# Kernel tuning notes

Measured on AMD Instinct MI355X. Metric: run time of the kernel, lower is better.

## Reference

```python
import jax, jax.numpy as jnp
import numpy as np

N = 100000
E = 1600000
NEG_SLOPE = 0.2


def _param(key, shape, scale=0.05):
    return jax.random.normal(key, shape, dtype=jnp.float32) * scale


def setup_inputs() -> dict:
    key = jax.random.key(0)
    ks = jax.random.split(key, 16)
    x = jax.random.normal(ks[0], (N, 128), dtype=jnp.float32)
    edge_index = jax.random.randint(ks[1], (2, E), 0, N, dtype=jnp.int64)
    # layer 1: 128 -> (H=2, C=64), concat
    W1 = _param(ks[2], (128, 2 * 64)); a_src1 = _param(ks[3], (2, 64)); a_dst1 = _param(ks[4], (2, 64)); b1 = jnp.zeros((128,), jnp.float32)
    # layer 2: 128 -> (H=2, C=64), concat
    W2 = _param(ks[5], (128, 2 * 64)); a_src2 = _param(ks[6], (2, 64)); a_dst2 = _param(ks[7], (2, 64)); b2 = jnp.zeros((128,), jnp.float32)
    # layer 3: 128 -> (H=1, C=64), mean (concat=False)
    W3 = _param(ks[8], (128, 1 * 64)); a_src3 = _param(ks[9], (1, 64)); a_dst3 = _param(ks[10], (1, 64)); b3 = jnp.zeros((64,), jnp.float32)
    return {"x": x, "edge_index": edge_index,
            "W1": W1, "a_src1": a_src1, "a_dst1": a_dst1, "b1": b1,
            "W2": W2, "a_src2": a_src2, "a_dst2": a_dst2, "b2": b2,
            "W3": W3, "a_src3": a_src3, "a_dst3": a_dst3, "b3": b3}


def gat_layer(x, src, dst, W, a_src, a_dst, b, concat):
    H, C = a_src.shape
    n = x.shape[0]
    h = (x @ W).reshape(n, H, C)                      # [N,H,C]
    # per-node attention logits (avoid [E,H,C] gather for the score step)
    al_s = jnp.sum(h * a_src[None], axis=-1)          # [N,H]
    al_d = jnp.sum(h * a_dst[None], axis=-1)          # [N,H]
    e = al_s[src] + al_d[dst]                         # [E',H]
    e = jnp.where(e > 0, e, NEG_SLOPE * e)            # LeakyReLU(0.2)
    # scatter-softmax over incoming edges per destination node
    m = jax.ops.segment_max(e, dst, num_segments=n)   # [N,H]
    ex = jnp.exp(e - m[dst])
    z = jax.ops.segment_sum(ex, dst, num_segments=n)  # [N,H]
    alpha = ex / z[dst]                               # [E',H]
    msg = h[src] * alpha[:, :, None]                  # [E',H,C]
    out = jax.ops.segment_sum(msg, dst, num_segments=n)  # [N,H,C]
    out = out.reshape(n, H * C) if concat else out.mean(axis=1)
    return out + b


def reference(x, edge_index, W1, a_src1, a_dst1, b1, W2, a_src2, a_dst2, b2, W3, a_src3, a_dst3, b3):
    n = x.shape[0]
    loop = jnp.arange(n, dtype=edge_index.dtype)
    src = jnp.concatenate([edge_index[0], loop])      # add self-loops (PyG default)
    dst = jnp.concatenate([edge_index[1], loop])
    h = gat_layer(x, src, dst, W1, a_src1, a_dst1, b1, True)
    h = jax.nn.relu(h)
    h = gat_layer(h, src, dst, W2, a_src2, a_dst2, b2, True)
    h = jax.nn.relu(h)
    return gat_layer(h, src, dst, W3, a_src3, a_dst3, b3, False)
```

## Files before the change

kernel.cpp:

```cpp
#include <hip/hip_runtime.h>

#define NEG_SLOPE 0.2f
#define BUK_SHIFT 9
#define BUK_SIZE 512
#define BUK_CAP 16384

typedef unsigned short u16;
typedef __attribute__((ext_vector_type(4))) float f4v;
typedef _Float16 h8 __attribute__((ext_vector_type(8)));

__device__ __forceinline__ u16 f2h_bits(_Float16 h) {
    union { _Float16 f; u16 u; } c;
    c.f = h;
    return c.u;
}


__device__ __forceinline__ void load_split_f32(const float* __restrict__ X, int row,
                                               int koff, int N, h8& hi, h8& lo) {
    float v[8];
    if (row < N) {
        float4 a = *(const float4*)&X[(size_t)row * 128 + koff];
        float4 b = *(const float4*)&X[(size_t)row * 128 + koff + 4];
        v[0] = a.x; v[1] = a.y; v[2] = a.z; v[3] = a.w;
        v[4] = b.x; v[5] = b.y; v[6] = b.z; v[7] = b.w;
    } else {
#pragma unroll
        for (int i = 0; i < 8; i++) v[i] = 0.f;
    }
    union { h8 s; _Float16 u[8]; } H, L;
#pragma unroll
    for (int i = 0; i < 8; i++) {
        H.u[i] = (_Float16)v[i];
        L.u[i] = (_Float16)(v[i] - (float)H.u[i]);
    }
    hi = H.s;
    lo = L.s;
}

template <int M, bool FP32X>
__device__ __forceinline__ void gemm_body(int gb, const float* __restrict__ Xf,
                                          const u16* __restrict__ XH,
                                          const u16* __restrict__ WTh,
                                          const u16* __restrict__ WTl,
                                          _Float16* __restrict__ Hout,
                                          float* __restrict__ als,
                                          float* __restrict__ ald, int nrows) {
    const int CT = M / 16;
    const int CTX = CT + 1;
    const int H = (M == 128) ? 2 : 1;
    int tid = threadIdx.x;
    int wv = tid >> 6, lane = tid & 63;
    int q = lane >> 4, nl = lane & 15;
    int R0 = gb * 256 + wv * 32;
    int rt0 = R0 >> 4;

    f4v acc[2][CTX];
    f4v z4 = {0.f, 0.f, 0.f, 0.f};
#pragma unroll
    for (int rt = 0; rt < 2; rt++)
#pragma unroll
        for (int ct = 0; ct < CTX; ct++) acc[rt][ct] = z4;

#pragma unroll
    for (int ch = 0; ch < 4; ch++) {
        h8 ah0, al0, ah1, al1;
        if (FP32X) {
            int koff = ch * 32 + q * 8;
            load_split_f32(Xf, R0 + nl, koff, nrows, ah0, al0);
            load_split_f32(Xf, R0 + 16 + nl, koff, nrows, ah1, al1);
        } else {
            size_t a0 = ((size_t)rt0 * 4 + ch) * 512 + lane * 8;
            size_t a1 = ((size_t)(rt0 + 1) * 4 + ch) * 512 + lane * 8;
            ah0 = *(const h8*)&XH[a0];
            ah1 = *(const h8*)&XH[a1];
        }
#pragma unroll
        for (int ct = 0; ct < CTX; ct++) {
            size_t bb = ((size_t)ct * 4 + ch) * 512 + lane * 8;
            h8 bh = *(const h8*)&WTh[bb];
            h8 bl = *(const h8*)&WTl[bb];
            acc[0][ct] = __builtin_amdgcn_mfma_f32_16x16x32_f16(ah0, bh, acc[0][ct], 0, 0, 0);
            acc[0][ct] = __builtin_amdgcn_mfma_f32_16x16x32_f16(ah0, bl, acc[0][ct], 0, 0, 0);
            acc[1][ct] = __builtin_amdgcn_mfma_f32_16x16x32_f16(ah1, bh, acc[1][ct], 0, 0, 0);
            acc[1][ct] = __builtin_amdgcn_mfma_f32_16x16x32_f16(ah1, bl, acc[1][ct], 0, 0, 0);
            if (FP32X) {
                acc[0][ct] = __builtin_amdgcn_mfma_f32_16x16x32_f16(al0, bh, acc[0][ct], 0, 0, 0);
                acc[1][ct] = __builtin_amdgcn_mfma_f32_16x16x32_f16(al1, bh, acc[1][ct], 0, 0, 0);
            }
        }
    }

#pragma unroll
    for (int rt = 0; rt < 2; rt++)
#pragma unroll
        for (int ct = 0; ct < CT; ct++)
#pragma unroll
            for (int r = 0; r < 4; r++) {
                int row = R0 + rt * 16 + q * 4 + r;
                if (row < nrows) Hout[(size_t)row * M + ct * 16 + nl] = (_Float16)acc[rt][ct][r];
            }

    if (nl < 2 * H) {
#pragma unroll
        for (int rt = 0; rt < 2; rt++)
#pragma unroll
            for (int r = 0; r < 4; r++) {
                int row = R0 + rt * 16 + q * 4 + r;
                if (row < nrows) {
                    float v = acc[rt][CT][r];
                    if (H == 2) {
                        float* dstp = (nl < 2) ? als : ald;
                        dstp[(size_t)row * 2 + (nl & 1)] = v;
                    } else {
                        float* dstp = (nl == 0) ? als : ald;
                        dstp[row] = v;
                    }
                }
            }
    }
}

template <int M, bool FP32X>
__launch_bounds__(512)
__global__ void k_gemm(const float* __restrict__ Xf, const u16* __restrict__ XH,
                       const u16* __restrict__ WTh, const u16* __restrict__ WTl,
                       _Float16* __restrict__ Hout, float* __restrict__ als,
                       float* __restrict__ ald, int nrows) {
    gemm_body<M, FP32X>(blockIdx.x, Xf, XH, WTh, WTl, Hout, als, ald, nrows);
}


__launch_bounds__(512)
__global__ void k_d1(const int* __restrict__ ei, int* g_cnt, int* buckets, int E, int nb,
                     int nbin, const float* __restrict__ W1, const float* __restrict__ as1,
                     const float* __restrict__ ad1, const float* __restrict__ W2,
                     const float* __restrict__ as2, const float* __restrict__ ad2,
                     const float* __restrict__ W3, const float* __restrict__ as3,
                     const float* __restrict__ ad3, u16* __restrict__ T1h,
                     u16* __restrict__ T1l, u16* __restrict__ T2h, u16* __restrict__ T2l,
                     u16* __restrict__ T3h, u16* __restrict__ T3l) {
    __shared__ int lcnt[256], lbase[256], lcur[256];
    int b = blockIdx.x;
    int t = threadIdx.x;
    if (b < nbin) {
        if (t < nb) {
            lcnt[t] = 0;
            lcur[t] = 0;
        }
        __syncthreads();
        int tile0 = b * 4096;
        int pk[8], bk[8];
#pragma unroll
        for (int k = 0; k < 8; k++) {
            int idx = tile0 + k * 512 + t;
            bk[k] = -1;
            if (idx < E) {
                int s = ei[idx];
                int d = ei[E + idx];
                bk[k] = d >> BUK_SHIFT;
                pk[k] = (s << BUK_SHIFT) | (d & (BUK_SIZE - 1));
                atomicAdd(&lcnt[bk[k]], 1);
            }
        }
        __syncthreads();
        if (t < nb && lcnt[t] > 0) lbase[t] = atomicAdd(&g_cnt[t], lcnt[t]);
        __syncthreads();
#pragma unroll
        for (int k = 0; k < 8; k++) {
            if (bk[k] >= 0) {
                int p = lbase[bk[k]] + atomicAdd(&lcur[bk[k]], 1);
                if (p < BUK_CAP) buckets[(bk[k] << 14) + p] = pk[k];
            }
        }
        return;
    }
    int rb = b - nbin;
    if (rb < 80) {
        int idx = rb * 512 + t;
        const float* W;
        u16 *Th, *Tl;
        int M, li;
        if (idx < 16384) {
            W = W1; Th = T1h; Tl = T1l; M = 128; li = idx;
        } else if (idx < 32768) {
            W = W2; Th = T2h; Tl = T2l; M = 128; li = idx - 16384;
        } else {
            W = W3; Th = T3h; Tl = T3l; M = 64; li = idx - 32768;
        }
        int c = li >> 7, k = li & 127;
        float v = W[(size_t)k * M + c];
        _Float16 h = (_Float16)v;
        _Float16 l = (_Float16)(v - (float)h);
        int ct = c >> 4, ch = k >> 5, q = (k >> 3) & 3, j = k & 7;
        size_t addr = ((size_t)ct * 4 + ch) * 512 + ((c & 15) + 16 * q) * 8 + j;
        Th[addr] = f2h_bits(h);
        Tl[addr] = f2h_bits(l);
    } else {
        int idx = (rb - 80) * 512 + t;
        if (idx >= 6144) return;
        int layer = idx >> 11;
        int rem = idx & 2047;
        int k = rem >> 4;
        int c = rem & 15;
        const float *W, *as, *ad;
        u16 *Th, *Tl;
        int M, CT, nc;
        if (layer == 0) {
            W = W1; as = as1; ad = ad1; Th = T1h; Tl = T1l; M = 128; CT = 8; nc = 4;
        } else if (layer == 1) {
            W = W2; as = as2; ad = ad2; Th = T2h; Tl = T2l; M = 128; CT = 8; nc = 4;
        } else {
            W = W3; as = as3; ad = ad3; Th = T3h; Tl = T3l; M = 64; CT = 4; nc = 2;
        }
        float val = 0.f;
        if (c < nc) {
            int side, hh;
            if (nc == 4) { side = c >> 1; hh = c & 1; }
            else { side = c; hh = 0; }
            const float* a = side ? ad : as;
            for (int j = 0; j < 64; j++)
                val += W[(size_t)k * M + hh * 64 + j] * a[hh * 64 + j];
        }
        _Float16 h = (_Float16)val;
        _Float16 l = (_Float16)(val - (float)h);
        int ch = k >> 5, q = (k >> 3) & 3, j = k & 7;
        size_t addr = ((size_t)CT * 4 + ch) * 512 + ((size_t)(c + 16 * q)) * 8 + j;
        Th[addr] = f2h_bits(h);
        Tl[addr] = f2h_bits(l);
    }
}


__launch_bounds__(512)
__global__ void k_d2(const int* __restrict__ g_cnt, const int* __restrict__ buckets,
                     int* csr_ptr, int* csr_src, int n, int nb,
                     const float* __restrict__ x, const u16* __restrict__ WTh,
                     const u16* __restrict__ WTl, _Float16* __restrict__ Hout,
                     float* __restrict__ als, float* __restrict__ ald) {
    __shared__ int lcnt[512], lsc[512], lcur[512], bsc[512];
    int b = blockIdx.x;
    int t = threadIdx.x;
    if (b >= nb) {
        gemm_body<128, true>(b - nb, x, nullptr, WTh, WTl, Hout, als, ald, n);
        return;
    }
    int nodes = min(BUK_SIZE, n - b * BUK_SIZE);
    int cnt = min(g_cnt[b], BUK_CAP);
    const int* bp = &buckets[b << 14];

    int bv = 0;
    if (t < nb) bv = min(g_cnt[t], BUK_CAP) + min(BUK_SIZE, n - t * BUK_SIZE);
    bsc[t] = bv;
    __syncthreads();
    for (int off = 1; off < 512; off <<= 1) {
        int xx = (t >= off) ? bsc[t - off] : 0;
        __syncthreads();
        bsc[t] += xx;
        __syncthreads();
    }
    int boff = bsc[b] - (cnt + nodes);
    int total = bsc[nb - 1];
    __syncthreads();

    lcnt[t] = 0;
    __syncthreads();
    for (int i = t; i < cnt; i += 512) atomicAdd(&lcnt[bp[i] & (BUK_SIZE - 1)], 1);
    __syncthreads();
    int myc = (t < nodes) ? (lcnt[t] + 1) : 0;
    lsc[t] = myc;
    __syncthreads();
    for (int off = 1; off < 512; off <<= 1) {
        int xx = (t >= off) ? lsc[t - off] : 0;
        __syncthreads();
        lsc[t] += xx;
        __syncthreads();
    }
    int excl = lsc[t] - myc;
    lcur[t] = excl;
    if (t < nodes) csr_ptr[b * BUK_SIZE + t] = boff + excl;
    if (b == nb - 1 && t == 0) csr_ptr[n] = total;
    __syncthreads();
    for (int i = t; i < cnt; i += 512) {
        int v = bp[i];
        int ld = v & (BUK_SIZE - 1);
        int p = atomicAdd(&lcur[ld], 1);
        csr_src[boff + p] = v >> BUK_SHIFT;
    }
    if (t < nodes) {
        int p = atomicAdd(&lcur[t], 1);
        csr_src[boff + p] = b * BUK_SIZE + t;
    }
}


__launch_bounds__(256)
__global__ void k_agg128(const int* __restrict__ ptr, const int* __restrict__ srcv,
                         const _Float16* __restrict__ Hh, const float* __restrict__ als,
                         const float* __restrict__ ald, const float* __restrict__ bias,
                         u16* __restrict__ OutX, int n) {
    int wvg = (blockIdx.x * blockDim.x + threadIdx.x) >> 6;
    int lane = threadIdx.x & 63;
    int nn = lane >> 4;
    int gl = lane & 15;
    int wid = wvg * 4 + nn;
    bool valid = wid < n;
    int widc = valid ? wid : (n - 1);
    int start = ptr[widc];
    int deg = valid ? (ptr[widc + 1] - start) : 0;
    int md = deg;
    md = max(md, __shfl_xor(md, 16));
    md = max(md, __shfl_xor(md, 32));
    float2 adv = *(const float2*)&ald[(size_t)widc * 2];
    int hsel = gl >> 3;
    int coff = gl * 8;
    float z0 = 0.f, z1 = 0.f;
    float acc[8];
#pragma unroll
    for (int c = 0; c < 8; c++) acc[c] = 0.f;

    for (int base = 0; base < md; base += 16) {
        int i = base + gl;
        int s_l = 0;
        float ex0 = 0.f, ex1 = 0.f;
        if (i < deg) {
            s_l = srcv[start + i];
            float2 av = *(const float2*)&als[(size_t)s_l * 2];
            float e0 = av.x + adv.x;
            e0 = e0 > 0.f ? e0 : NEG_SLOPE * e0;
            ex0 = __expf(e0);
            float e1 = av.y + adv.y;
            e1 = e1 > 0.f ? e1 : NEG_SLOPE * e1;
            ex1 = __expf(e1);
        }
        z0 += ex0;
        z1 += ex1;
        int cnt = min(16, md - base);
        for (int jp = 0; jp < cnt; jp += 4) {
            int nk = min(4, cnt - jp);
            h8 hv[4];
            float w[4];
#pragma unroll
            for (int k = 0; k < 4; k++) {
                if (k < nk) {
                    int j = nn * 16 + jp + k;
                    int s = __shfl(s_l, j);
                    float w0 = __shfl(ex0, j);
                    float w1 = __shfl(ex1, j);
                    w[k] = hsel ? w1 : w0;
                    hv[k] = *(const h8*)&Hh[(size_t)s * 128 + coff];
                }
            }
#pragma unroll
            for (int k = 0; k < 4; k++) {
                if (k < nk) {
#pragma unroll
                    for (int c = 0; c < 8; c++)
                        acc[c] = fmaf(w[k], (float)hv[k][c], acc[c]);
                }
            }
        }
    }

#pragma unroll
    for (int m = 1; m <= 8; m <<= 1) {
        z0 += __shfl_xor(z0, m);
        z1 += __shfl_xor(z1, m);
    }
    if (valid) {
        float zinv = hsel ? (1.f / z1) : (1.f / z0);
        float4 b0 = *(const float4*)&bias[coff];
        float4 b1 = *(const float4*)&bias[coff + 4];
        float bb[8] = {b0.x, b0.y, b0.z, b0.w, b1.x, b1.y, b1.z, b1.w};
        union { _Float16 f[8]; h8 v; } O;
#pragma unroll
        for (int c = 0; c < 8; c++) {
            float o = fmaxf(fmaf(acc[c], zinv, bb[c]), 0.f);
            O.f[c] = (_Float16)o;
        }
        int ch = coff >> 5, qq = (coff >> 3) & 3;
        size_t tb = ((size_t)(wid >> 4) * 4 + ch) * 512 + ((size_t)((wid & 15) + 16 * qq)) * 8;
        *(h8*)&OutX[tb] = O.v;
    }
}


__launch_bounds__(256)
__global__ void k_agg64(const int* __restrict__ ptr, const int* __restrict__ srcv,
                        const _Float16* __restrict__ Hh, const float* __restrict__ als,
                        const float* __restrict__ ald, const float* __restrict__ bias,
                        float* __restrict__ Out, int n) {
    int wvg = (blockIdx.x * blockDim.x + threadIdx.x) >> 6;
    int lane = threadIdx.x & 63;
    int nn = lane >> 3;
    int gl = lane & 7;
    int wid = wvg * 8 + nn;
    bool valid = wid < n;
    int widc = valid ? wid : (n - 1);
    int start = ptr[widc];
    int deg = valid ? (ptr[widc + 1] - start) : 0;
    int md = deg;
    md = max(md, __shfl_xor(md, 8));
    md = max(md, __shfl_xor(md, 16));
    md = max(md, __shfl_xor(md, 32));
    float ad0 = ald[widc];
    int coff = gl * 8;
    float z = 0.f;
    float acc[8];
#pragma unroll
    for (int c = 0; c < 8; c++) acc[c] = 0.f;

    for (int base = 0; base < md; base += 8) {
        int i = base + gl;
        int s_l = 0;
        float ex0 = 0.f;
        if (i < deg) {
            s_l = srcv[start + i];
            float e = als[s_l] + ad0;
            e = e > 0.f ? e : NEG_SLOPE * e;
            ex0 = __expf(e);
        }
        z += ex0;
        int cnt = min(8, md - base);
        for (int jp = 0; jp < cnt; jp += 4) {
            int nk = min(4, cnt - jp);
            h8 hv[4];
            float w[4];
#pragma unroll
            for (int k = 0; k < 4; k++) {
                if (k < nk) {
                    int j = nn * 8 + jp + k;
                    int s = __shfl(s_l, j);
                    w[k] = __shfl(ex0, j);
                    hv[k] = *(const h8*)&Hh[(size_t)s * 64 + coff];
                }
            }
#pragma unroll
            for (int k = 0; k < 4; k++) {
                if (k < nk) {
#pragma unroll
                    for (int c = 0; c < 8; c++)
                        acc[c] = fmaf(w[k], (float)hv[k][c], acc[c]);
                }
            }
        }
    }

#pragma unroll
    for (int m = 1; m <= 4; m <<= 1) z += __shfl_xor(z, m);
    if (valid) {
        float zinv = 1.f / z;
        float4 b0 = *(const float4*)&bias[coff];
        float4 b1 = *(const float4*)&bias[coff + 4];
        float4 o1, o2;
        o1.x = fmaf(acc[0], zinv, b0.x);
        o1.y = fmaf(acc[1], zinv, b0.y);
        o1.z = fmaf(acc[2], zinv, b0.z);
        o1.w = fmaf(acc[3], zinv, b0.w);
        o2.x = fmaf(acc[4], zinv, b1.x);
        o2.y = fmaf(acc[5], zinv, b1.y);
        o2.z = fmaf(acc[6], zinv, b1.z);
        o2.w = fmaf(acc[7], zinv, b1.w);
        *(float4*)&Out[(size_t)wid * 64 + coff] = o1;
        *(float4*)&Out[(size_t)wid * 64 + coff + 4] = o2;
    }
}


extern "C" void kernel_launch(void* const* d_in, const int* in_sizes, int n_in,
                              void* d_out, int out_size, void* d_ws, size_t ws_size,
                              hipStream_t stream) {
    const float* x = (const float*)d_in[0];
    const int* ei = (const int*)d_in[1];
    const float* W1 = (const float*)d_in[2];
    const float* as1 = (const float*)d_in[3];
    const float* ad1 = (const float*)d_in[4];
    const float* b1 = (const float*)d_in[5];
    const float* W2 = (const float*)d_in[6];
    const float* as2 = (const float*)d_in[7];
    const float* ad2 = (const float*)d_in[8];
    const float* b2 = (const float*)d_in[9];
    const float* W3 = (const float*)d_in[10];
    const float* as3 = (const float*)d_in[11];
    const float* ad3 = (const float*)d_in[12];
    const float* b3 = (const float*)d_in[13];

    const int N = in_sizes[0] / 128;
    const int E = in_sizes[1] / 2;
    const int NB = (N + BUK_SIZE - 1) / BUK_SIZE;
    const int Npad = (N + 255) & ~255;

    char* p = (char*)d_ws;
    auto alloc = [&](size_t bytes) -> char* {
        char* r = p;
        p += (bytes + 255) & ~(size_t)255;
        return r;
    };
    int* g_cnt = (int*)alloc(256 * 4);
    int* buckets = (int*)alloc((size_t)NB * BUK_CAP * 4);
    int* csr_ptr = (int*)alloc((size_t)(N + 1) * 4);
    int* csr_src = (int*)alloc((size_t)(E + N) * 4);
    float* als = (float*)alloc((size_t)N * 2 * 4);
    float* aldv = (float*)alloc((size_t)N * 2 * 4);
    _Float16* Hbuf = (_Float16*)alloc((size_t)N * 128 * 2);
    u16* XH = (u16*)alloc((size_t)Npad * 128 * 2);
    u16* WT1h = (u16*)alloc(9 * 2048 * 2);
    u16* WT1l = (u16*)alloc(9 * 2048 * 2);
    u16* WT2h = (u16*)alloc(9 * 2048 * 2);
    u16* WT2l = (u16*)alloc(9 * 2048 * 2);
    u16* WT3h = (u16*)alloc(5 * 2048 * 2);
    u16* WT3l = (u16*)alloc(5 * 2048 * 2);

    const int GTOT = Npad / 256;
    const int NBIN = (E + 4095) / 4096;
    const int waves128 = (N + 3) / 4;
    const int nbAgg128 = (waves128 + 3) / 4;
    const int waves64 = (N + 7) / 8;
    const int nbAgg64 = (waves64 + 3) / 4;

    hipMemsetAsync(g_cnt, 0, 256 * 4, stream);

    k_d1<<<NBIN + 92, 512, 0, stream>>>(ei, g_cnt, buckets, E, NB, NBIN,
                                        W1, as1, ad1, W2, as2, ad2, W3, as3, ad3,
                                        WT1h, WT1l, WT2h, WT2l, WT3h, WT3l);

    k_d2<<<NB + GTOT, 512, 0, stream>>>(g_cnt, buckets, csr_ptr, csr_src, N, NB,
                                        x, WT1h, WT1l, Hbuf, als, aldv);

    k_agg128<<<nbAgg128, 256, 0, stream>>>(csr_ptr, csr_src, Hbuf, als, aldv, b1, XH, N);

    k_gemm<128, false><<<GTOT, 512, 0, stream>>>(nullptr, XH, WT2h, WT2l,
                                                 Hbuf, als, aldv, N);
    k_agg128<<<nbAgg128, 256, 0, stream>>>(csr_ptr, csr_src, Hbuf, als, aldv, b2, XH, N);

    k_gemm<64, false><<<GTOT, 512, 0, stream>>>(nullptr, XH, WT3h, WT3l,
                                                Hbuf, als, aldv, N);
    k_agg64<<<nbAgg64, 256, 0, stream>>>(csr_ptr, csr_src, Hbuf, als, aldv, b3,
                                         (float*)d_out, N);
}
```

Measured before the change: 400.5 us.

## Fuse all GAT stages into one cooperative persistent kernel with grid syncs

Replaces the memset and seven separate launches with a single cooperative kernel that loops over virtual blocks for each stage and uses grid.sync between stages, falling back to per-stage kernels if the cooperative launch fails. This targets launch overhead and inter-kernel gaps. The aggregation kernels are also recast as 512-thread blocks, and the gather inner loop is widened from 4 to 8 neighbours per batch. The risks are lower occupancy from the merged kernel's register and LDS footprint, grid-sync costs, and load imbalance across the persistent grid.

```diff
diff --git a/kernel.cpp b/kernel.cpp
--- a/kernel.cpp
+++ b/kernel.cpp
@@ -1,4 +1,7 @@
 #include <hip/hip_runtime.h>
+#include <hip/hip_cooperative_groups.h>
+
+namespace cg = cooperative_groups;
 
 #define NEG_SLOPE 0.2f
 #define BUK_SHIFT 9
@@ -9,10 +12,172 @@
 typedef __attribute__((ext_vector_type(4))) float f4v;
 typedef _Float16 h8 __attribute__((ext_vector_type(8)));
 
+struct MegaP {
+    const float* x;
+    const int* ei;
+    const float *W1, *as1, *ad1, *b1;
+    const float *W2, *as2, *ad2, *b2;
+    const float *W3, *as3, *ad3, *b3;
+    float* out;
+    int N, E, NB, NBIN, GTOT, VB128, VB64;
+    int *g_cnt, *buckets, *csr_ptr, *csr_src;
+    float *als, *ald;
+    _Float16* Hbuf;
+    u16* XH;
+    u16 *WT1h, *WT1l, *WT2h, *WT2l, *WT3h, *WT3l;
+};
+
 __device__ __forceinline__ u16 f2h_bits(_Float16 h) {
     union { _Float16 f; u16 u; } c;
     c.f = h;
     return c.u;
+}
+
+
+__device__ void wsplit_role(const MegaP& p, int idx) {
+    const float* W;
+    u16 *Th, *Tl;
+    int M, li;
+    if (idx < 16384) {
+        W = p.W1; Th = p.WT1h; Tl = p.WT1l; M = 128; li = idx;
+    } else if (idx < 32768) {
+        W = p.W2; Th = p.WT2h; Tl = p.WT2l; M = 128; li = idx - 16384;
+    } else {
+        W = p.W3; Th = p.WT3h; Tl = p.WT3l; M = 64; li = idx - 32768;
+    }
+    int c = li >> 7, k = li & 127;
+    float v = W[(size_t)k * M + c];
+    _Float16 h = (_Float16)v;
+    _Float16 l = (_Float16)(v - (float)h);
+    int ct = c >> 4, ch = k >> 5, q = (k >> 3) & 3, j = k & 7;
+    size_t addr = ((size_t)ct * 4 + ch) * 512 + ((c & 15) + 16 * q) * 8 + j;
+    Th[addr] = f2h_bits(h);
+    Tl[addr] = f2h_bits(l);
+}
+
+__device__ void wa_role(const MegaP& p, int idx) {
+    if (idx >= 6144) return;
+    int layer = idx >> 11;
+    int rem = idx & 2047;
+    int k = rem >> 4;
+    int c = rem & 15;
+    const float *W, *as, *ad;
+    u16 *Th, *Tl;
+    int M, CT, nc;
+    if (layer == 0) {
+        W = p.W1; as = p.as1; ad = p.ad1; Th = p.WT1h; Tl = p.WT1l; M = 128; CT = 8; nc = 4;
+    } else if (layer == 1) {
+        W = p.W2; as = p.as2; ad = p.ad2; Th = p.WT2h; Tl = p.WT2l; M = 128; CT = 8; nc = 4;
+    } else {
+        W = p.W3; as = p.as3; ad = p.ad3; Th = p.WT3h; Tl = p.WT3l; M = 64; CT = 4; nc = 2;
+    }
+    float val = 0.f;
+    if (c < nc) {
+        int side, hh;
+        if (nc == 4) { side = c >> 1; hh = c & 1; }
+        else { side = c; hh = 0; }
+        const float* a = side ? ad : as;
+        for (int j = 0; j < 64; j++)
+            val += W[(size_t)k * M + hh * 64 + j] * a[hh * 64 + j];
+    }
+    _Float16 h = (_Float16)val;
+    _Float16 l = (_Float16)(val - (float)h);
+    int ch = k >> 5, q = (k >> 3) & 3, j = k & 7;
+    size_t addr = ((size_t)CT * 4 + ch) * 512 + ((size_t)(c + 16 * q)) * 8 + j;
+    Th[addr] = f2h_bits(h);
+    Tl[addr] = f2h_bits(l);
+}
+
+__device__ void binscatter_role(const MegaP& p, int b, int t, int* smem) {
+    int* lcnt = smem;
+    int* lbase = smem + 256;
+    int* lcur = smem + 512;
+    int nb = p.NB;
+    if (t < nb) {
+        lcnt[t] = 0;
+        lcur[t] = 0;
+    }
+    __syncthreads();
+    int tile0 = b * 4096;
+    int pk[8], bk[8];
+#pragma unroll
+    for (int k = 0; k < 8; k++) {
+        int idx = tile0 + k * 512 + t;
+        bk[k] = -1;
+        if (idx < p.E) {
+            int s = p.ei[idx];
+            int d = p.ei[p.E + idx];
+            bk[k] = d >> BUK_SHIFT;
+            pk[k] = (s << BUK_SHIFT) | (d & (BUK_SIZE - 1));
+            atomicAdd(&lcnt[bk[k]], 1);
+        }
+    }
+    __syncthreads();
+    if (t < nb && lcnt[t] > 0) lbase[t] = atomicAdd(&p.g_cnt[t], lcnt[t]);
+    __syncthreads();
+#pragma unroll
+    for (int k = 0; k < 8; k++) {
+        if (bk[k] >= 0) {
+            int pos = lbase[bk[k]] + atomicAdd(&lcur[bk[k]], 1);
+            if (pos < BUK_CAP) p.buckets[(bk[k] << 14) + pos] = pk[k];
+        }
+    }
+    __syncthreads();
+}
+
+__device__ void csr_role(const MegaP& p, int b, int t, int* smem) {
+    int* lcnt = smem;
+    int* lsc = smem + 512;
+    int* lcur = smem + 1024;
+    int* bsc = smem + 1536;
+    int n = p.N, nb = p.NB;
+    int nodes = min(BUK_SIZE, n - b * BUK_SIZE);
+    int cnt = min(p.g_cnt[b], BUK_CAP);
+    const int* bp = &p.buckets[b << 14];
+
+    int bv = 0;
+    if (t < nb) bv = min(p.g_cnt[t], BUK_CAP) + min(BUK_SIZE, n - t * BUK_SIZE);
+    bsc[t] = bv;
+    __syncthreads();
+    for (int off = 1; off < 512; off <<= 1) {
+        int xx = (t >= off) ? bsc[t - off] : 0;
+        __syncthreads();
+        bsc[t] += xx;
+        __syncthreads();
+    }
+    int boff = bsc[b] - (cnt + nodes);
+    int total = bsc[nb - 1];
+    __syncthreads();
+
+    lcnt[t] = 0;
+    __syncthreads();
+    for (int i = t; i < cnt; i += 512) atomicAdd(&lcnt[bp[i] & (BUK_SIZE - 1)], 1);
+    __syncthreads();
+    int myc = (t < nodes) ? (lcnt[t] + 1) : 0;
+    lsc[t] = myc;
+    __syncthreads();
+    for (int off = 1; off < 512; off <<= 1) {
+        int xx = (t >= off) ? lsc[t - off] : 0;
+        __syncthreads();
+        lsc[t] += xx;
+        __syncthreads();
+    }
+    int excl = lsc[t] - myc;
+    lcur[t] = excl;
+    if (t < nodes) p.csr_ptr[b * BUK_SIZE + t] = boff + excl;
+    if (b == nb - 1 && t == 0) p.csr_ptr[n] = total;
+    __syncthreads();
+    for (int i = t; i < cnt; i += 512) {
+        int v = bp[i];
+        int ld = v & (BUK_SIZE - 1);
+        int pos = atomicAdd(&lcur[ld], 1);
+        p.csr_src[boff + pos] = v >> BUK_SHIFT;
+    }
+    if (t < nodes) {
+        int pos = atomicAdd(&lcur[t], 1);
+        p.csr_src[boff + pos] = b * BUK_SIZE + t;
+    }
+    __syncthreads();
 }
 
 
@@ -39,13 +204,10 @@
 }
 
 template <int M, bool FP32X>
-__device__ __forceinline__ void gemm_body(int gb, const float* __restrict__ Xf,
-                                          const u16* __restrict__ XH,
-                                          const u16* __restrict__ WTh,
-                                          const u16* __restrict__ WTl,
-                                          _Float16* __restrict__ Hout,
-                                          float* __restrict__ als,
-                                          float* __restrict__ ald, int nrows) {
+__device__ void gemm_body(int gb, const float* __restrict__ Xf, const u16* __restrict__ XH,
+                          const u16* __restrict__ WTh, const u16* __restrict__ WTl,
+                          _Float16* __restrict__ Hout, float* __restrict__ als,
+                          float* __restrict__ ald, int nrows) {
     const int CT = M / 16;
     const int CTX = CT + 1;
     const int H = (M == 128) ? 2 : 1;
@@ -121,197 +283,22 @@
     }
 }
 
-template <int M, bool FP32X>
-__launch_bounds__(512)
-__global__ void k_gemm(const float* __restrict__ Xf, const u16* __restrict__ XH,
-                       const u16* __restrict__ WTh, const u16* __restrict__ WTl,
-                       _Float16* __restrict__ Hout, float* __restrict__ als,
-                       float* __restrict__ ald, int nrows) {
-    gemm_body<M, FP32X>(blockIdx.x, Xf, XH, WTh, WTl, Hout, als, ald, nrows);
-}
-
-
-__launch_bounds__(512)
-__global__ void k_d1(const int* __restrict__ ei, int* g_cnt, int* buckets, int E, int nb,
-                     int nbin, const float* __restrict__ W1, const float* __restrict__ as1,
-                     const float* __restrict__ ad1, const float* __restrict__ W2,
-                     const float* __restrict__ as2, const float* __restrict__ ad2,
-                     const float* __restrict__ W3, const float* __restrict__ as3,
-                     const float* __restrict__ ad3, u16* __restrict__ T1h,
-                     u16* __restrict__ T1l, u16* __restrict__ T2h, u16* __restrict__ T2l,
-                     u16* __restrict__ T3h, u16* __restrict__ T3l) {
-    __shared__ int lcnt[256], lbase[256], lcur[256];
-    int b = blockIdx.x;
-    int t = threadIdx.x;
-    if (b < nbin) {
-        if (t < nb) {
-            lcnt[t] = 0;
-            lcur[t] = 0;
-        }
-        __syncthreads();
-        int tile0 = b * 4096;
-        int pk[8], bk[8];
-#pragma unroll
-        for (int k = 0; k < 8; k++) {
-            int idx = tile0 + k * 512 + t;
-            bk[k] = -1;
-            if (idx < E) {
-                int s = ei[idx];
-                int d = ei[E + idx];
-                bk[k] = d >> BUK_SHIFT;
-                pk[k] = (s << BUK_SHIFT) | (d & (BUK_SIZE - 1));
-                atomicAdd(&lcnt[bk[k]], 1);
-            }
-        }
-        __syncthreads();
-        if (t < nb && lcnt[t] > 0) lbase[t] = atomicAdd(&g_cnt[t], lcnt[t]);
-        __syncthreads();
-#pragma unroll
-        for (int k = 0; k < 8; k++) {
-            if (bk[k] >= 0) {
-                int p = lbase[bk[k]] + atomicAdd(&lcur[bk[k]], 1);
-                if (p < BUK_CAP) buckets[(bk[k] << 14) + p] = pk[k];
-            }
-        }
-        return;
-    }
-    int rb = b - nbin;
-    if (rb < 80) {
-        int idx = rb * 512 + t;
-        const float* W;
-        u16 *Th, *Tl;
-        int M, li;
-        if (idx < 16384) {
-            W = W1; Th = T1h; Tl = T1l; M = 128; li = idx;
-        } else if (idx < 32768) {
-            W = W2; Th = T2h; Tl = T2l; M = 128; li = idx - 16384;
-        } else {
-            W = W3; Th = T3h; Tl = T3l; M = 64; li = idx - 32768;
-        }
-        int c = li >> 7, k = li & 127;
-        float v = W[(size_t)k * M + c];
-        _Float16 h = (_Float16)v;
-        _Float16 l = (_Float16)(v - (float)h);
-        int ct = c >> 4, ch = k >> 5, q = (k >> 3) & 3, j = k & 7;
-        size_t addr = ((size_t)ct * 4 + ch) * 512 + ((c & 15) + 16 * q) * 8 + j;
-        Th[addr] = f2h_bits(h);
-        Tl[addr] = f2h_bits(l);
-    } else {
-        int idx = (rb - 80) * 512 + t;
-        if (idx >= 6144) return;
-        int layer = idx >> 11;
-        int rem = idx & 2047;
-        int k = rem >> 4;
-        int c = rem & 15;
-        const float *W, *as, *ad;
-        u16 *Th, *Tl;
-        int M, CT, nc;
-        if (layer == 0) {
-            W = W1; as = as1; ad = ad1; Th = T1h; Tl = T1l; M = 128; CT = 8; nc = 4;
-        } else if (layer == 1) {
-            W = W2; as = as2; ad = ad2; Th = T2h; Tl = T2l; M = 128; CT = 8; nc = 4;
-        } else {
-            W = W3; as = as3; ad = ad3; Th = T3h; Tl = T3l; M = 64; CT = 4; nc = 2;
-        }
-        float val = 0.f;
-        if (c < nc) {
-            int side, hh;
-            if (nc == 4) { side = c >> 1; hh = c & 1; }
-            else { side = c; hh = 0; }
-            const float* a = side ? ad : as;
-            for (int j = 0; j < 64; j++)
-                val += W[(size_t)k * M + hh * 64 + j] * a[hh * 64 + j];
-        }
-        _Float16 h = (_Float16)val;
-        _Float16 l = (_Float16)(val - (float)h);
-        int ch = k >> 5, q = (k >> 3) & 3, j = k & 7;
-        size_t addr = ((size_t)CT * 4 + ch) * 512 + ((size_t)(c + 16 * q)) * 8 + j;
-        Th[addr] = f2h_bits(h);
-        Tl[addr] = f2h_bits(l);
-    }
-}
-
-
-__launch_bounds__(512)
-__global__ void k_d2(const int* __restrict__ g_cnt, const int* __restrict__ buckets,
-                     int* csr_ptr, int* csr_src, int n, int nb,
-                     const float* __restrict__ x, const u16* __restrict__ WTh,
-                     const u16* __restrict__ WTl, _Float16* __restrict__ Hout,
-                     float* __restrict__ als, float* __restrict__ ald) {
-    __shared__ int lcnt[512], lsc[512], lcur[512], bsc[512];
-    int b = blockIdx.x;
-    int t = threadIdx.x;
-    if (b >= nb) {
-        gemm_body<128, true>(b - nb, x, nullptr, WTh, WTl, Hout, als, ald, n);
-        return;
-    }
-    int nodes = min(BUK_SIZE, n - b * BUK_SIZE);
-    int cnt = min(g_cnt[b], BUK_CAP);
-    const int* bp = &buckets[b << 14];
-
-    int bv = 0;
-    if (t < nb) bv = min(g_cnt[t], BUK_CAP) + min(BUK_SIZE, n - t * BUK_SIZE);
-    bsc[t] = bv;
-    __syncthreads();
-    for (int off = 1; off < 512; off <<= 1) {
-        int xx = (t >= off) ? bsc[t - off] : 0;
-        __syncthreads();
-        bsc[t] += xx;
-        __syncthreads();
-    }
-    int boff = bsc[b] - (cnt + nodes);
-    int total = bsc[nb - 1];
-    __syncthreads();
-
-    lcnt[t] = 0;
-    __syncthreads();
-    for (int i = t; i < cnt; i += 512) atomicAdd(&lcnt[bp[i] & (BUK_SIZE - 1)], 1);
-    __syncthreads();
-    int myc = (t < nodes) ? (lcnt[t] + 1) : 0;
-    lsc[t] = myc;
-    __syncthreads();
-    for (int off = 1; off < 512; off <<= 1) {
-        int xx = (t >= off) ? lsc[t - off] : 0;
-        __syncthreads();
-        lsc[t] += xx;
-        __syncthreads();
-    }
-    int excl = lsc[t] - myc;
-    lcur[t] = excl;
-    if (t < nodes) csr_ptr[b * BUK_SIZE + t] = boff + excl;
-    if (b == nb - 1 && t == 0) csr_ptr[n] = total;
-    __syncthreads();
-    for (int i = t; i < cnt; i += 512) {
-        int v = bp[i];
-        int ld = v & (BUK_SIZE - 1);
-        int p = atomicAdd(&lcur[ld], 1);
-        csr_src[boff + p] = v >> BUK_SHIFT;
-    }
-    if (t < nodes) {
-        int p = atomicAdd(&lcur[t], 1);
-        csr_src[boff + p] = b * BUK_SIZE + t;
-    }
-}
-
-
-__launch_bounds__(256)
-__global__ void k_agg128(const int* __restrict__ ptr, const int* __restrict__ srcv,
-                         const _Float16* __restrict__ Hh, const float* __restrict__ als,
-                         const float* __restrict__ ald, const float* __restrict__ bias,
-                         u16* __restrict__ OutX, int n) {
-    int wvg = (blockIdx.x * blockDim.x + threadIdx.x) >> 6;
-    int lane = threadIdx.x & 63;
+
+__device__ void agg128_role(const MegaP& p, int t, int vb, const float* __restrict__ bias) {
+    int wv = t >> 6, lane = t & 63;
+    int wvg = vb * 8 + wv;
+    if (wvg * 4 >= p.N) return;
     int nn = lane >> 4;
     int gl = lane & 15;
     int wid = wvg * 4 + nn;
-    bool valid = wid < n;
-    int widc = valid ? wid : (n - 1);
-    int start = ptr[widc];
-    int deg = valid ? (ptr[widc + 1] - start) : 0;
+    bool valid = wid < p.N;
+    int widc = valid ? wid : (p.N - 1);
+    int start = p.csr_ptr[widc];
+    int deg = valid ? (p.csr_ptr[widc + 1] - start) : 0;
     int md = deg;
     md = max(md, __shfl_xor(md, 16));
     md = max(md, __shfl_xor(md, 32));
-    float2 adv = *(const float2*)&ald[(size_t)widc * 2];
+    float2 adv = *(const float2*)&p.ald[(size_t)widc * 2];
     int hsel = gl >> 3;
     int coff = gl * 8;
     float z0 = 0.f, z1 = 0.f;
@@ -324,8 +311,8 @@
         int s_l = 0;
         float ex0 = 0.f, ex1 = 0.f;
         if (i < deg) {
-            s_l = srcv[start + i];
-            float2 av = *(const float2*)&als[(size_t)s_l * 2];
+            s_l = p.csr_src[start + i];
+            float2 av = *(const float2*)&p.als[(size_t)s_l * 2];
             float e0 = av.x + adv.x;
             e0 = e0 > 0.f ? e0 : NEG_SLOPE * e0;
             ex0 = __expf(e0);
@@ -336,23 +323,23 @@
         z0 += ex0;
         z1 += ex1;
         int cnt = min(16, md - base);
-        for (int jp = 0; jp < cnt; jp += 4) {
-            int nk = min(4, cnt - jp);
-            h8 hv[4];
-            float w[4];
-#pragma unroll
-            for (int k = 0; k < 4; k++) {
+        for (int jp = 0; jp < cnt; jp += 8) {
+            int nk = min(8, cnt - jp);
+            h8 hv[8];
+            float w[8];
+#pragma unroll
+            for (int k = 0; k < 8; k++) {
                 if (k < nk) {
                     int j = nn * 16 + jp + k;
                     int s = __shfl(s_l, j);
                     float w0 = __shfl(ex0, j);
                     float w1 = __shfl(ex1, j);
                     w[k] = hsel ? w1 : w0;
-                    hv[k] = *(const h8*)&Hh[(size_t)s * 128 + coff];
+                    hv[k] = *(const h8*)&p.Hbuf[(size_t)s * 128 + coff];
                 }
             }
 #pragma unroll
-            for (int k = 0; k < 4; k++) {
+            for (int k = 0; k < 8; k++) {
                 if (k < nk) {
 #pragma unroll
                     for (int c = 0; c < 8; c++)
@@ -380,30 +367,26 @@
         }
         int ch = coff >> 5, qq = (coff >> 3) & 3;
         size_t tb = ((size_t)(wid >> 4) * 4 + ch) * 512 + ((size_t)((wid & 15) + 16 * qq)) * 8;
-        *(h8*)&OutX[tb] = O.v;
-    }
-}
-
-
-__launch_bounds__(256)
-__global__ void k_agg64(const int* __restrict__ ptr, const int* __restrict__ srcv,
-                        const _Float16* __restrict__ Hh, const float* __restrict__ als,
-                        const float* __restrict__ ald, const float* __restrict__ bias,
-                        float* __restrict__ Out, int n) {
-    int wvg = (blockIdx.x * blockDim.x + threadIdx.x) >> 6;
-    int lane = threadIdx.x & 63;
+        *(h8*)&p.XH[tb] = O.v;
+    }
+}
+
+__device__ void agg64_role(const MegaP& p, int t, int vb) {
+    int wv = t >> 6, lane = t & 63;
+    int wvg = vb * 8 + wv;
+    if (wvg * 8 >= p.N) return;
     int nn = lane >> 3;
     int gl = lane & 7;
     int wid = wvg * 8 + nn;
-    bool valid = wid < n;
-    int widc = valid ? wid : (n - 1);
-    int start = ptr[widc];
-    int deg = valid ? (ptr[widc + 1] - start) : 0;
+    bool valid = wid < p.N;
+    int widc = valid ? wid : (p.N - 1);
+    int start = p.csr_ptr[widc];
+    int deg = valid ? (p.csr_ptr[widc + 1] - start) : 0;
     int md = deg;
     md = max(md, __shfl_xor(md, 8));
     md = max(md, __shfl_xor(md, 16));
     md = max(md, __shfl_xor(md, 32));
-    float ad0 = ald[widc];
+    float ad0 = p.ald[widc];
     int coff = gl * 8;
     float z = 0.f;
     float acc[8];
@@ -415,33 +398,30 @@
         int s_l = 0;
         float ex0 = 0.f;
         if (i < deg) {
-            s_l = srcv[start + i];
-            float e = als[s_l] + ad0;
+            s_l = p.csr_src[start + i];
+            float e = p.als[s_l] + ad0;
             e = e > 0.f ? e : NEG_SLOPE * e;
             ex0 = __expf(e);
         }
         z += ex0;
         int cnt = min(8, md - base);
-        for (int jp = 0; jp < cnt; jp += 4) {
-            int nk = min(4, cnt - jp);
-            h8 hv[4];
-            float w[4];
-#pragma unroll
-            for (int k = 0; k < 4; k++) {
-                if (k < nk) {
-                    int j = nn * 8 + jp + k;
-                    int s = __shfl(s_l, j);
-                    w[k] = __shfl(ex0, j);
-                    hv[k] = *(const h8*)&Hh[(size_t)s * 64 + coff];
-                }
+        h8 hv[8];
+        float w[8];
+#pragma unroll
+        for (int k = 0; k < 8; k++) {
+            if (k < cnt) {
+                int j = nn * 8 + k;
+                int s = __shfl(s_l, j);
+                w[k] = __shfl(ex0, j);
+                hv[k] = *(const h8*)&p.Hbuf[(size_t)s * 64 + coff];
             }
-#pragma unroll
-            for (int k = 0; k < 4; k++) {
-                if (k < nk) {
-#pragma unroll
-                    for (int c = 0; c < 8; c++)
-                        acc[c] = fmaf(w[k], (float)hv[k][c], acc[c]);
-                }
+        }
+#pragma unroll
+        for (int k = 0; k < 8; k++) {
+            if (k < cnt) {
+#pragma unroll
+                for (int c = 0; c < 8; c++)
+                    acc[c] = fmaf(w[k], (float)hv[k][c], acc[c]);
             }
         }
     }
@@ -450,8 +430,8 @@
     for (int m = 1; m <= 4; m <<= 1) z += __shfl_xor(z, m);
     if (valid) {
         float zinv = 1.f / z;
-        float4 b0 = *(const float4*)&bias[coff];
-        float4 b1 = *(const float4*)&bias[coff + 4];
+        float4 b0 = *(const float4*)&p.b3[coff];
+        float4 b1 = *(const float4*)&p.b3[coff + 4];
         float4 o1, o2;
         o1.x = fmaf(acc[0], zinv, b0.x);
         o1.y = fmaf(acc[1], zinv, b0.y);
@@ -461,34 +441,123 @@
         o2.y = fmaf(acc[5], zinv, b1.y);
         o2.z = fmaf(acc[6], zinv, b1.z);
         o2.w = fmaf(acc[7], zinv, b1.w);
-        *(float4*)&Out[(size_t)wid * 64 + coff] = o1;
-        *(float4*)&Out[(size_t)wid * 64 + coff + 4] = o2;
-    }
+        *(float4*)&p.out[(size_t)wid * 64 + coff] = o1;
+        *(float4*)&p.out[(size_t)wid * 64 + coff + 4] = o2;
+    }
+}
+
+
+__global__ __launch_bounds__(512, 4) void mega(MegaP p) {
+    __shared__ int smem[2048];
+    cg::grid_group grid = cg::this_grid();
+    int t = threadIdx.x;
+
+    for (int vb = blockIdx.x; vb < 93; vb += gridDim.x) {
+        if (vb == 0) {
+            if (t < 256) p.g_cnt[t] = 0;
+        } else if (vb < 81) {
+            wsplit_role(p, (vb - 1) * 512 + t);
+        } else {
+            wa_role(p, (vb - 81) * 512 + t);
+        }
+    }
+    __threadfence();
+    grid.sync();
+    for (int vb = blockIdx.x; vb < p.NBIN; vb += gridDim.x) binscatter_role(p, vb, t, smem);
+    __threadfence();
+    grid.sync();
+    for (int vb = blockIdx.x; vb < p.NB + p.GTOT; vb += gridDim.x) {
+        if (vb < p.NB)
+            csr_role(p, vb, t, smem);
+        else
+            gemm_body<128, true>(vb - p.NB, p.x, nullptr, p.WT1h, p.WT1l, p.Hbuf, p.als,
+                                 p.ald, p.N);
+    }
+    __threadfence();
+    grid.sync();
+    for (int vb = blockIdx.x; vb < p.VB128; vb += gridDim.x) agg128_role(p, t, vb, p.b1);
+    __threadfence();
+    grid.sync();
+    for (int vb = blockIdx.x; vb < p.GTOT; vb += gridDim.x)
+        gemm_body<128, false>(vb, nullptr, p.XH, p.WT2h, p.WT2l, p.Hbuf, p.als, p.ald, p.N);
+    __threadfence();
+    grid.sync();
+    for (int vb = blockIdx.x; vb < p.VB128; vb += gridDim.x) agg128_role(p, t, vb, p.b2);
+    __threadfence();
+    grid.sync();
+    for (int vb = blockIdx.x; vb < p.GTOT; vb += gridDim.x)
+        gemm_body<64, false>(vb, nullptr, p.XH, p.WT3h, p.WT3l, p.Hbuf, p.als, p.ald, p.N);
+    __threadfence();
+    grid.sync();
+    for (int vb = blockIdx.x; vb < p.VB64; vb += gridDim.x) agg64_role(p, t, vb);
+}
+
+
+__launch_bounds__(512) __global__ void k_f0(MegaP p) {
+    int vb = blockIdx.x, t = threadIdx.x;
+    if (vb == 0) {
+        if (t < 256) p.g_cnt[t] = 0;
+    } else if (vb < 81) {
+        wsplit_role(p, (vb - 1) * 512 + t);
+    } else {
+        wa_role(p, (vb - 81) * 512 + t);
+    }
+}
+__launch_bounds__(512) __global__ void k_f1(MegaP p) {
+    __shared__ int smem[2048];
+    binscatter_role(p, blockIdx.x, threadIdx.x, smem);
+}
+__launch_bounds__(512) __global__ void k_f2(MegaP p) {
+    __shared__ int smem[2048];
+    int vb = blockIdx.x;
+    if (vb < p.NB)
+        csr_role(p, vb, threadIdx.x, smem);
+    else
+        gemm_body<128, true>(vb - p.NB, p.x, nullptr, p.WT1h, p.WT1l, p.Hbuf, p.als, p.ald,
+                             p.N);
+}
+__launch_bounds__(512) __global__ void k_f3(MegaP p, const float* bias) {
+    agg128_role(p, threadIdx.x, blockIdx.x, bias);
+}
+template <int M>
+__launch_bounds__(512) __global__ void k_f4(MegaP p, const u16* Th, const u16* Tl) {
+    gemm_body<M, false>(blockIdx.x, nullptr, p.XH, Th, Tl, p.Hbuf, p.als, p.ald, p.N);
+}
+__launch_bounds__(512) __global__ void k_f7(MegaP p) {
+    agg64_role(p, threadIdx.x, blockIdx.x);
 }
 
 
 extern "C" void kernel_launch(void* const* d_in, const int* in_sizes, int n_in,
                               void* d_out, int out_size, void* d_ws, size_t ws_size,
                               hipStream_t stream) {
-    const float* x = (const float*)d_in[0];
-    const int* ei = (const int*)d_in[1];
-    const float* W1 = (const float*)d_in[2];
-    const float* as1 = (const float*)d_in[3];
-    const float* ad1 = (const float*)d_in[4];
-    const float* b1 = (const float*)d_in[5];
-    const float* W2 = (const float*)d_in[6];
-    const float* as2 = (const float*)d_in[7];
-    const float* ad2 = (const float*)d_in[8];
-    const float* b2 = (const float*)d_in[9];
-    const float* W3 = (const float*)d_in[10];
-    const float* as3 = (const float*)d_in[11];
-    const float* ad3 = (const float*)d_in[12];
-    const float* b3 = (const float*)d_in[13];
+    MegaP P;
+    P.x = (const float*)d_in[0];
+    P.ei = (const int*)d_in[1];
+    P.W1 = (const float*)d_in[2];
+    P.as1 = (const float*)d_in[3];
+    P.ad1 = (const float*)d_in[4];
+    P.b1 = (const float*)d_in[5];
+    P.W2 = (const float*)d_in[6];
+    P.as2 = (const float*)d_in[7];
+    P.ad2 = (const float*)d_in[8];
+    P.b2 = (const float*)d_in[9];
+    P.W3 = (const float*)d_in[10];
+    P.as3 = (const float*)d_in[11];
+    P.ad3 = (const float*)d_in[12];
+    P.b3 = (const float*)d_in[13];
+    P.out = (float*)d_out;
 
     const int N = in_sizes[0] / 128;
     const int E = in_sizes[1] / 2;
-    const int NB = (N + BUK_SIZE - 1) / BUK_SIZE;
+    P.N = N;
+    P.E = E;
+    P.NB = (N + BUK_SIZE - 1) / BUK_SIZE;
+    P.NBIN = (E + 4095) / 4096;
     const int Npad = (N + 255) & ~255;
+    P.GTOT = Npad / 256;
+    P.VB128 = ((N + 3) / 4 + 7) / 8;
+    P.VB64 = ((N + 7) / 8 + 7) / 8;
 
     char* p = (char*)d_ws;
     auto alloc = [&](size_t bytes) -> char* {
@@ -496,45 +565,52 @@
         p += (bytes + 255) & ~(size_t)255;
         return r;
     };
-    int* g_cnt = (int*)alloc(256 * 4);
-    int* buckets = (int*)alloc((size_t)NB * BUK_CAP * 4);
-    int* csr_ptr = (int*)alloc((size_t)(N + 1) * 4);
-    int* csr_src = (int*)alloc((size_t)(E + N) * 4);
-    float* als = (float*)alloc((size_t)N * 2 * 4);
-    float* aldv = (float*)alloc((size_t)N * 2 * 4);
-    _Float16* Hbuf = (_Float16*)alloc((size_t)N * 128 * 2);
-    u16* XH = (u16*)alloc((size_t)Npad * 128 * 2);
-    u16* WT1h = (u16*)alloc(9 * 2048 * 2);
-    u16* WT1l = (u16*)alloc(9 * 2048 * 2);
-    u16* WT2h = (u16*)alloc(9 * 2048 * 2);
-    u16* WT2l = (u16*)alloc(9 * 2048 * 2);
-    u16* WT3h = (u16*)alloc(5 * 2048 * 2);
-    u16* WT3l = (u16*)alloc(5 * 2048 * 2);
-
-    const int GTOT = Npad / 256;
-    const int NBIN = (E + 4095) / 4096;
-    const int waves128 = (N + 3) / 4;
-    const int nbAgg128 = (waves128 + 3) / 4;
-    const int waves64 = (N + 7) / 8;
-    const int nbAgg64 = (waves64 + 3) / 4;
-
-    hipMemsetAsync(g_cnt, 0, 256 * 4, stream);
-
-    k_d1<<<NBIN + 92, 512, 0, stream>>>(ei, g_cnt, buckets, E, NB, NBIN,
-                                        W1, as1, ad1, W2, as2, ad2, W3, as3, ad3,
-                                        WT1h, WT1l, WT2h, WT2l, WT3h, WT3l);
-
-    k_d2<<<NB + GTOT, 512, 0, stream>>>(g_cnt, buckets, csr_ptr, csr_src, N, NB,
-                                        x, WT1h, WT1l, Hbuf, als, aldv);
-
-    k_agg128<<<nbAgg128, 256, 0, stream>>>(csr_ptr, csr_src, Hbuf, als, aldv, b1, XH, N);
-
-    k_gemm<128, false><<<GTOT, 512, 0, stream>>>(nullptr, XH, WT2h, WT2l,
-                                                 Hbuf, als, aldv, N);
-    k_agg128<<<nbAgg128, 256, 0, stream>>>(csr_ptr, csr_src, Hbuf, als, aldv, b2, XH, N);
-
-    k_gemm<64, false><<<GTOT, 512, 0, stream>>>(nullptr, XH, WT3h, WT3l,
-                                                Hbuf, als, aldv, N);
-    k_agg64<<<nbAgg64, 256, 0, stream>>>(csr_ptr, csr_src, Hbuf, als, aldv, b3,
-                                         (float*)d_out, N);
-}
+    P.g_cnt = (int*)alloc(256 * 4);
+    P.buckets = (int*)alloc((size_t)P.NB * BUK_CAP * 4);
+    P.csr_ptr = (int*)alloc((size_t)(N + 1) * 4);
+    P.csr_src = (int*)alloc((size_t)(E + N) * 4);
+    P.als = (float*)alloc((size_t)N * 2 * 4);
+    P.ald = (float*)alloc((size_t)N * 2 * 4);
+    P.Hbuf = (_Float16*)alloc((size_t)N * 128 * 2);
+    P.XH = (u16*)alloc((size_t)Npad * 128 * 2);
+    P.WT1h = (u16*)alloc(9 * 2048 * 2);
+    P.WT1l = (u16*)alloc(9 * 2048 * 2);
+    P.WT2h = (u16*)alloc(9 * 2048 * 2);
+    P.WT2l = (u16*)alloc(9 * 2048 * 2);
+    P.WT3h = (u16*)alloc(5 * 2048 * 2);
+    P.WT3l = (u16*)alloc(5 * 2048 * 2);
+
+    static int nblk = -2;
+    if (nblk == -2) {
+        int mb = 0, dev = 0, ncu = 0;
+        hipError_t e1 = hipGetDevice(&dev);
+        hipError_t e2 = hipOccupancyMaxActiveBlocksPerMultiprocessor(&mb, mega, 512, 0);
+        hipError_t e3 =
+            hipDeviceGetAttribute(&ncu, hipDeviceAttributeMultiprocessorCount, dev);
+        if (e1 == hipSuccess && e2 == hipSuccess && e3 == hipSuccess && mb > 0 && ncu > 0)
+            nblk = mb * ncu;
+        else
+            nblk = 0;
+    }
+
+    bool done = false;
+    if (nblk > 0) {
+        int g = nblk < P.VB128 ? nblk : P.VB128;
+        void* args[] = {(void*)&P};
+        if (hipLaunchCooperativeKernel((const void*)mega, dim3(g), dim3(512), args, 0,
+                                       stream) == hipSuccess)
+            done = true;
+        else
+            nblk = 0;
+    }
+    if (!done) {
+        k_f0<<<93, 512, 0, stream>>>(P);
+        k_f1<<<P.NBIN, 512, 0, stream>>>(P);
+        k_f2<<<P.NB + P.GTOT, 512, 0, stream>>>(P);
+        k_f3<<<P.VB128, 512, 0, stream>>>(P, P.b1);
+        k_f4<128><<<P.GTOT, 512, 0, stream>>>(P, P.WT2h, P.WT2l);
+        k_f3<<<P.VB128, 512, 0, stream>>>(P, P.b2);
+        k_f4<64><<<P.GTOT, 512, 0, stream>>>(P, P.WT3h, P.WT3l);
+        k_f7<<<P.VB64, 512, 0, stream>>>(P);
+    }
+}
```

Result: slower. 444.2 us (+10.9%).
